# Kernel tuning notes

Hardware: AMD Instinct MI355X
Metric: run time of the kernel (lower is better)

## Reference

```python
import jax, jax.numpy as jnp
import numpy as np

B, T = 4096, 2048
CLIP = 1.0e5


def _hv(x):
    # smooth Heaviside: ~0 for x<0, ~1 for x>0
    return (jnp.tanh(5.0 * x) + 1.0) * 0.5


def setup_inputs() -> dict:
    key = jax.random.key(0)
    k1, _ = jax.random.split(key)
    # columns: prcp, tmean, dayl (all in [0,1) like normalized forcings)
    inputs = jax.random.uniform(k1, (B, T, 3), dtype=jnp.float32)
    # 15 scalar bucket parameters, all initialized to 0.5 as in build():
    # f, smax, qmax, ddf, tmin, tmax, Kc, SCmax, spmax, qpmax, kp, sgmax, qgmax, Kl, Kn
    theta = jnp.full((15,), 0.5, dtype=jnp.float32)
    return {"inputs": inputs, "theta": theta}


def _run(inputs, theta):
    f, smax, qmax, ddf, tmin, tmax, Kc, SCmax, spmax, qpmax, kp, sgmax, qgmax, Kl, Kn = [
        theta[i] for i in range(15)
    ]
    prcp = inputs[:, :, 0]   # [B,T]
    tmean = inputs[:, :, 1]
    dayl = inputs[:, :, 2]
    # Hamon-style PET computed once for the whole sequence
    pet = 29.8 * (dayl * 24.0) * 0.611 * jnp.exp(17.3 * tmean / (tmean + 237.3)) / (tmean + 273.2)

    # rescaled parameters (done once; constant over time)
    f_ = f / 10.0
    smax_ = smax * 1950.0
    qmax_ = qmax * 50.0
    ddf_ = ddf * 5.0
    tmin_ = tmin * -3.0
    tmax_ = tmax * 3.0
    Kc_ = Kc * 0.5
    SCmax_ = SCmax * 1.5
    spmax_ = spmax * 1950.0
    qpmax_ = qpmax * 40.0
    sgmax_ = sgmax * 1950.0
    qgmax_ = qgmax * 40.0
    Kl_ = Kl * 0.5
    Kn_ = Kn * 0.5
    Dc = 0.986 * 0.862

    def step(state, xt):
        s0, s1, s2, s3, s4 = [state[:, i] for i in range(5)]  # each [B]
        p, t, dl, pe = xt  # each [B]

        # canopy bucket
        day = _hv(dl - 0.5)
        night = _hv(0.5 - dl)
        scmax_t = day * SCmax_ * 2.0 + night * SCmax_ * 0.6
        lai_t = day * 0.478 + night * 0.15
        kc_t = day * Kc_ + night * Kc_ * 0.4
        pintc = (_hv(p - 0.1) * _hv(s0) * _hv(s0 - scmax_t) * p
                 + _hv(p - 0.1) * _hv(scmax_t - s0) * kc_t * Dc * lai_t)

        # rain/snow partition
        psnow = _hv(tmin_ - t) * p
        prain = _hv(t - tmin_) * p

        # snow bucket
        melt = _hv(t - tmax_) * _hv(s1) * jnp.minimum(s1, ddf_ * (t - tmax_))

        # preferential bucket
        qpref = (_hv(s2) * _hv(s2 - spmax_) * qpmax_
                 + _hv(s2) * _hv(spmax_ - s2) * kp * p * jnp.exp(-f_ * (spmax_ - s2)))

        # capillary (soil) bucket
        et = (_hv(s3) * _hv(s3 - smax_) * pe
              + _hv(s3) * _hv(smax_ - s3) * pe * (s3 / smax_))
        qsub = (_hv(s3) * _hv(s3 - smax_) * qmax_
                + _hv(s3) * _hv(smax_ - s3) * qmax_ * jnp.exp(-f_ * (smax_ - s3)))
        qout = _hv(s3) * _hv(s3 - smax_) * (s3 - smax_)

        # gravity bucket
        qslow = (_hv(s4) * _hv(s4 - sgmax_) * qgmax_
                 + _hv(s4) * _hv(sgmax_ - s4) * (p * Kl_ + p * p * Kn_) * jnp.exp(-f_ * (sgmax_ - s4)))

        ns0 = s0 + jnp.clip(pintc, -CLIP, CLIP)
        ns1 = s1 + jnp.clip(psnow - melt, -CLIP, CLIP)
        ns2 = s2 + jnp.clip(qpref, -CLIP, CLIP)
        ns3 = s3 + jnp.clip(prain + melt - et - qsub - qout, -CLIP, CLIP)
        ns4 = s4 + jnp.clip(qslow, -CLIP, CLIP)
        new_state = jnp.stack([ns0, ns1, ns2, ns3, ns4], axis=1)  # [B,5]
        return new_state, new_state

    init = jnp.zeros((inputs.shape[0], 5), dtype=inputs.dtype)
    xs = (prcp.T, tmean.T, dayl.T, pet.T)  # time-major [T,B]
    _, seq = jax.lax.scan(step, init, xs)  # seq: [T,B,5]
    return jnp.transpose(seq, (1, 0, 2))  # [B,T,5] state trajectories


def reference(inputs, theta):
    return _run(inputs, theta)
```

## Files before the change

### kernel.cpp

```cpp
#include <hip/hip_runtime.h>


#define NB 4096
#define NT 2048
#define CHUNK 32
#define NCHUNK (NT / CHUNK)
#define K1 16
#define NCH1 (NT / K1)
#define BT ((size_t)NB * (size_t)NT)

#define L2E10 14.4269504089f
#define L2E    1.44269504089f

__device__ __forceinline__ float rcpf(float x) { return __builtin_amdgcn_rcpf(x); }
__device__ __forceinline__ float ex2(float a)  { return __builtin_amdgcn_exp2f(a); }
__device__ __forceinline__ float ex2c(float a) { return __builtin_amdgcn_exp2f(fminf(a, 80.0f)); }
__device__ __forceinline__ float clip1e5(float x) {
    return __builtin_amdgcn_fmed3f(x, -100000.0f, 100000.0f);
}
__device__ __forceinline__ void pinbuf(const float* d, int n4) {
    const float4* v = (const float4*)d;
    #pragma unroll
    for (int i = 0; i < n4; ++i)
        asm volatile("" :: "v"(v[i].x), "v"(v[i].y), "v"(v[i].z), "v"(v[i].w));
}

__global__ __launch_bounds__(256)
void pre_kernel(const float* __restrict__ inp, const float* __restrict__ theta,
                float* __restrict__ scr) {
    const float ddf_  = theta[3] * 5.0f;
    const float tmin_ = theta[4] * -3.0f;
    const float tmax_ = theta[5] * 3.0f;
    const float c_sn  = -L2E10 * tmin_;
    const float c_m   =  L2E10 * tmax_;
    const float c_dd  = -ddf_ * tmax_;

    const size_t k = (size_t)blockIdx.x * 256 + threadIdx.x;
    const float p  = inp[k * 3 + 0];
    const float tm = inp[k * 3 + 1];
    const float dl = inp[k * 3 + 2];

    const float A1 = tm + 237.3f;
    const float A2 = tm + 273.2f;
    const float q  = rcpf(A1 * A2);
    const float pe = 436.98672f * dl * ex2(24.958624f * tm * (q * A2)) * (q * A1);
    const float psnow = rcpf(1.0f + ex2(fmaf(L2E10, tm, c_sn))) * p;
    const float prain = p - psnow;
    const float dm  = 1.0f + ex2(fmaf(-L2E10, tm, c_m));
    const float mdd = fmaf(ddf_, tm, c_dd);

    scr[0 * BT + k] = pe;
    scr[1 * BT + k] = psnow;
    scr[2 * BT + k] = prain;
    scr[3 * BT + k] = dm;
    scr[4 * BT + k] = mdd;
}

__global__ __launch_bounds__(64, 1)
void prnn_roles(const float* __restrict__ inp, const float* __restrict__ theta,
                float* __restrict__ out, float* __restrict__ wsp, int use_ws) {
    const int lane = threadIdx.x;
    const int role = blockIdx.x & 3;
    const int b = (blockIdx.x >> 2) * 64 + lane;

    const float f_     = theta[0] * 0.1f;
    const float smax_  = theta[1] * 1950.0f;
    const float qmax_  = theta[2] * 50.0f;
    const float ddf_   = theta[3] * 5.0f;
    const float tmin_  = theta[4] * -3.0f;
    const float tmax_  = theta[5] * 3.0f;
    const float Kc_    = theta[6] * 0.5f;
    const float SCmax_ = theta[7] * 1.5f;
    const float spmax_ = theta[8] * 1950.0f;
    const float qpmax_ = theta[9] * 40.0f;
    const float kp     = theta[10];
    const float sgmax_ = theta[11] * 1950.0f;
    const float qgmax_ = theta[12] * 40.0f;
    const float Kl_    = theta[13] * 0.5f;
    const float Kn_    = theta[14] * 0.5f;

    const float inv_smax = rcpf(smax_);
    const float KcDc  = Kc_ * 0.849932f;
    const float c_sn  = -L2E10 * tmin_;
    const float c_m   =  L2E10 * tmax_;
    const float c_dd  = -ddf_ * tmax_;
    const float c_sc1 =  L2E10 * SCmax_ * 1.4f;
    const float c_sc0 =  L2E10 * SCmax_ * 0.6f;
    const float c_2p  =  L2E10 * spmax_;
    const float c_3s  =  L2E10 * smax_;
    const float c_4s  =  L2E10 * sgmax_;
    const float fE    = f_ * L2E;
    const float c_E2  = -fE * spmax_;
    const float c_E3  = -fE * smax_;
    const float c_E4  = -fE * sgmax_;

    const float* ip = inp + (size_t)b * (NT * 3);
    float*       op = out + (size_t)b * (NT * 5);
    float* wbase = use_ws ? wsp : out;

    auto plane_storeN = [&](float* plane, const float* ob, int off, int n4) {
        float4* d = (float4*)(plane + (size_t)off);
        const float4* s = (const float4*)ob;
        #pragma unroll
        for (int i = 0; i < 8; ++i) { if (i < n4) d[i] = s[i]; }
    };

    if (role == 0) {
        float s0 = 0.f;
        float bA[CHUNK * 3], bB[CHUNK * 3];
        float* w0 = wbase + 0 * BT + (size_t)b * NT;
        auto pf = [&](float* d, int c) {
            const float4* s = (const float4*)(ip + (size_t)c * (CHUNK * 3));
            #pragma unroll
            for (int i = 0; i < (CHUNK * 3) / 4; ++i) ((float4*)d)[i] = s[i];
        };
        auto cw = [&](const float* d, int c) {
            float ob[CHUNK];
            #pragma unroll
            for (int i = 0; i < CHUNK; ++i) {
                const float p  = d[i * 3 + 0];
                const float dl = d[i * 3 + 2];
                const float day = rcpf(1.0f + ex2(fmaf(-L2E10, dl, 7.21347520f)));
                const float da  = 1.0f + ex2(fmaf(-L2E10, p, L2E));
                const float lai   = fmaf(0.328f, day, 0.15f);
                const float kcf   = fmaf(0.6f, day, 0.4f);
                const float kterm = KcDc * kcf * lai;
                const float zday  = fmaf(c_sc1, day, c_sc0);
                const float e0  = ex2(-L2E10 * s0);
                const float esc = ex2(fmaf(-L2E10, s0, zday));
                const float d0  = 1.0f + e0;
                const float dsc = 1.0f + esc;
                const float Rp  = rcpf(da * d0 * dsc);
                const float pintc = Rp * fmaf(d0 * esc, kterm, p);
                s0 += clip1e5(pintc);
                ob[i] = s0;
            }
            if (use_ws) plane_storeN(w0, ob, c * CHUNK, CHUNK / 4);
            else {
                #pragma unroll
                for (int i = 0; i < CHUNK; ++i) op[(c * CHUNK + i) * 5 + 0] = ob[i];
            }
        };
        pf(bA, 0);
        for (int c = 0; c < NCHUNK; c += 2) {
            pf(bB, c + 1);
            pinbuf(bA, (CHUNK * 3) / 4);
            cw(bA, c);
            if (c + 2 < NCHUNK) pf(bA, c + 2);
            pinbuf(bB, (CHUNK * 3) / 4);
            cw(bB, c + 1);
        }
    } else if (role == 1) {
        float s1 = 0.f, s3 = 0.f;
        float* w1 = wbase + 1 * BT + (size_t)b * NT;
        float* w3 = wbase + 3 * BT + (size_t)b * NT;
        if (use_ws) {
            const float* PE = out + 0 * BT + (size_t)b * NT;
            const float* PS = out + 1 * BT + (size_t)b * NT;
            const float* PR = out + 2 * BT + (size_t)b * NT;
            const float* DM = out + 3 * BT + (size_t)b * NT;
            const float* MD = out + 4 * BT + (size_t)b * NT;
            float peA[K1], psA[K1], prA[K1], dmA[K1], mdA[K1];
            float peB[K1], psB[K1], prB[K1], dmB[K1], mdB[K1];
            float ob1[2 * K1], ob3[2 * K1];
            auto pf = [&](float* pe_, float* ps_, float* pr_, float* dm_,
                          float* md_, int c) {
                const int o = c * K1;
                #pragma unroll
                for (int i = 0; i < K1 / 4; ++i) {
                    ((float4*)pe_)[i] = *(const float4*)(PE + o + i * 4);
                    ((float4*)ps_)[i] = *(const float4*)(PS + o + i * 4);
                    ((float4*)pr_)[i] = *(const float4*)(PR + o + i * 4);
                    ((float4*)dm_)[i] = *(const float4*)(DM + o + i * 4);
                    ((float4*)md_)[i] = *(const float4*)(MD + o + i * 4);
                }
            };
            auto pin5 = [&](const float* pe_, const float* ps_, const float* pr_,
                            const float* dm_, const float* md_) {
                pinbuf(pe_, K1 / 4); pinbuf(ps_, K1 / 4); pinbuf(pr_, K1 / 4);
                pinbuf(dm_, K1 / 4); pinbuf(md_, K1 / 4);
            };
            auto cw = [&](const float* pe_, const float* ps_, const float* pr_,
                          const float* dm_, const float* md_, int half) {
                #pragma unroll
                for (int i = 0; i < K1; ++i) {
                    const float pe = pe_[i], psnow = ps_[i], prain = pr_[i];
                    const float dm = dm_[i], mdd = md_[i];
                    const float e1 = ex2(-L2E10 * s1);
                    const float melt = rcpf(dm * (1.0f + e1)) * fminf(s1, mdd);
                    const float e3  = ex2(-L2E10 * s3);
                    const float e3s = ex2c(fmaf(-L2E10, s3, c_3s));
                    const float R3  = rcpf((1.0f + e3) * (1.0f + e3s));
                    const float E3  = ex2(fmaf(fE, s3, c_E3));
                    const float t_et = pe * fmaf(e3s * s3, inv_smax, 1.0f);
                    const float t_qs = qmax_ * fmaf(e3s, E3, 1.0f);
                    const float outflux = R3 * (t_et + t_qs + (s3 - smax_));
                    const float ds3 = prain + melt - outflux;
                    s1 += clip1e5(psnow - melt);
                    s3 += clip1e5(ds3);
                    ob1[half * K1 + i] = s1;
                    ob3[half * K1 + i] = s3;
                }
            };
            pf(peA, psA, prA, dmA, mdA, 0);
            for (int c = 0; c < NCH1; c += 2) {
                pf(peB, psB, prB, dmB, mdB, c + 1);
                pin5(peA, psA, prA, dmA, mdA);
                cw(peA, psA, prA, dmA, mdA, 0);
                if (c + 2 < NCH1) pf(peA, psA, prA, dmA, mdA, c + 2);
                pin5(peB, psB, prB, dmB, mdB);
                cw(peB, psB, prB, dmB, mdB, 1);
                plane_storeN(w1, ob1, c * K1, (2 * K1) / 4);
                plane_storeN(w3, ob3, c * K1, (2 * K1) / 4);
            }
        } else {
            float bA[CHUNK * 3], bB[CHUNK * 3];
            auto pf = [&](float* d, int c) {
                const float4* s = (const float4*)(ip + (size_t)c * (CHUNK * 3));
                #pragma unroll
                for (int i = 0; i < (CHUNK * 3) / 4; ++i) ((float4*)d)[i] = s[i];
            };
            auto cw = [&](const float* d, int c) {
                #pragma unroll
                for (int i = 0; i < CHUNK; ++i) {
                    const float p  = d[i * 3 + 0];
                    const float tm = d[i * 3 + 1];
                    const float dl = d[i * 3 + 2];
                    const float A1 = tm + 237.3f;
                    const float A2 = tm + 273.2f;
                    const float qq = rcpf(A1 * A2);
                    const float pe = 436.98672f * dl * ex2(24.958624f * tm * (qq * A2)) * (qq * A1);
                    const float psnow = rcpf(1.0f + ex2(fmaf(L2E10, tm, c_sn))) * p;
                    const float dm = 1.0f + ex2(fmaf(-L2E10, tm, c_m));
                    const float prain = p - psnow;
                    const float e1 = ex2(-L2E10 * s1);
                    const float melt = rcpf(dm * (1.0f + e1))
                                       * fminf(s1, fmaf(ddf_, tm, c_dd));
                    const float e3  = ex2(-L2E10 * s3);
                    const float e3s = ex2c(fmaf(-L2E10, s3, c_3s));
                    const float R3  = rcpf((1.0f + e3) * (1.0f + e3s));
                    const float E3  = ex2(fmaf(fE, s3, c_E3));
                    const float t_et = pe * fmaf(e3s * s3, inv_smax, 1.0f);
                    const float t_qs = qmax_ * fmaf(e3s, E3, 1.0f);
                    const float outflux = R3 * (t_et + t_qs + (s3 - smax_));
                    const float ds3 = prain + melt - outflux;
                    s1 += clip1e5(psnow - melt);
                    s3 += clip1e5(ds3);
                    const int t = c * CHUNK + i;
                    op[t * 5 + 1] = s1;
                    op[t * 5 + 3] = s3;
                }
            };
            pf(bA, 0);
            for (int c = 0; c < NCHUNK; c += 2) {
                pf(bB, c + 1);
                pinbuf(bA, (CHUNK * 3) / 4);
                cw(bA, c);
                if (c + 2 < NCHUNK) pf(bA, c + 2);
                pinbuf(bB, (CHUNK * 3) / 4);
                cw(bB, c + 1);
            }
        }
    } else if (role == 2) {
        float s2 = 0.f;
        float pA[CHUNK], pB[CHUNK];
        float* w2 = wbase + 2 * BT + (size_t)b * NT;
        auto pf = [&](float* P, int c) {
            #pragma unroll
            for (int i = 0; i < CHUNK; ++i) P[i] = ip[(c * CHUNK + i) * 3 + 0];
        };
        auto cw = [&](const float* P, int c) {
            float ob[CHUNK];
            #pragma unroll
            for (int i = 0; i < CHUNK; ++i) {
                const float p = P[i];
                const float e2  = ex2(-L2E10 * s2);
                const float e2p = ex2c(fmaf(-L2E10, s2, c_2p));
                const float R2  = rcpf((1.0f + e2) * (1.0f + e2p));
                const float E2  = ex2(fmaf(fE, s2, c_E2));
                const float qpref = R2 * fmaf(e2p * E2, kp * p, qpmax_);
                s2 += clip1e5(qpref);
                ob[i] = s2;
            }
            if (use_ws) plane_storeN(w2, ob, c * CHUNK, CHUNK / 4);
            else {
                #pragma unroll
                for (int i = 0; i < CHUNK; ++i) op[(c * CHUNK + i) * 5 + 2] = ob[i];
            }
        };
        pf(pA, 0);
        for (int c = 0; c < NCHUNK; c += 2) {
            pf(pB, c + 1);
            pinbuf(pA, CHUNK / 4);
            cw(pA, c);
            if (c + 2 < NCHUNK) pf(pA, c + 2);
            pinbuf(pB, CHUNK / 4);
            cw(pB, c + 1);
        }
    } else {
        float s4 = 0.f;
        float pA[CHUNK], pB[CHUNK];
        float* w4 = wbase + 4 * BT + (size_t)b * NT;
        auto pf = [&](float* P, int c) {
            #pragma unroll
            for (int i = 0; i < CHUNK; ++i) P[i] = ip[(c * CHUNK + i) * 3 + 0];
        };
        auto cw = [&](const float* P, int c) {
            float ob[CHUNK];
            #pragma unroll
            for (int i = 0; i < CHUNK; ++i) {
                const float p = P[i];
                const float e4  = ex2(-L2E10 * s4);
                const float e4s = ex2c(fmaf(-L2E10, s4, c_4s));
                const float R4  = rcpf((1.0f + e4) * (1.0f + e4s));
                const float E4  = ex2(fmaf(fE, s4, c_E4));
                const float pl  = p * fmaf(p, Kn_, Kl_);
                const float qslow = R4 * fmaf(e4s * E4, pl, qgmax_);
                s4 += clip1e5(qslow);
                ob[i] = s4;
            }
            if (use_ws) plane_storeN(w4, ob, c * CHUNK, CHUNK / 4);
            else {
                #pragma unroll
                for (int i = 0; i < CHUNK; ++i) op[(c * CHUNK + i) * 5 + 4] = ob[i];
            }
        };
        pf(pA, 0);
        for (int c = 0; c < NCHUNK; c += 2) {
            pf(pB, c + 1);
            pinbuf(pA, CHUNK / 4);
            cw(pA, c);
            if (c + 2 < NCHUNK) pf(pA, c + 2);
            pinbuf(pB, CHUNK / 4);
            cw(pB, c + 1);
        }
    }
}

__global__ __launch_bounds__(256)
void tx_kernel(const float* __restrict__ wsp, float* __restrict__ out) {
    const size_t idx = (size_t)blockIdx.x * 256 + threadIdx.x;
    const size_t b  = idx / (NT / 4);
    const size_t t0 = (idx % (NT / 4)) * 4;
    const float* base = wsp + b * NT + t0;
    const float4 v0 = *(const float4*)(base + 0 * BT);
    const float4 v1 = *(const float4*)(base + 1 * BT);
    const float4 v2 = *(const float4*)(base + 2 * BT);
    const float4 v3 = *(const float4*)(base + 3 * BT);
    const float4 v4 = *(const float4*)(base + 4 * BT);
    float4* o = (float4*)(out + (b * NT + t0) * 5);
    o[0] = make_float4(v0.x, v1.x, v2.x, v3.x);
    o[1] = make_float4(v4.x, v0.y, v1.y, v2.y);
    o[2] = make_float4(v3.y, v4.y, v0.z, v1.z);
    o[3] = make_float4(v2.z, v3.z, v4.z, v0.w);
    o[4] = make_float4(v1.w, v2.w, v3.w, v4.w);
}

extern "C" void kernel_launch(void* const* d_in, const int* in_sizes, int n_in,
                              void* d_out, int out_size, void* d_ws, size_t ws_size,
                              hipStream_t stream) {
    const float* inp   = (const float*)d_in[0];
    const float* theta = (const float*)d_in[1];
    float* out = (float*)d_out;
    float* wsp = (float*)d_ws;
    const int use_ws = (wsp != nullptr && ws_size >= 5 * sizeof(float) * BT) ? 1 : 0;
    if (use_ws)
        pre_kernel<<<(int)(BT / 256), 256, 0, stream>>>(inp, theta, out);
    prnn_roles<<<4 * (NB / 64), 64, 0, stream>>>(inp, theta, out, wsp, use_ws);
    if (use_ws)
        tx_kernel<<<(int)(BT / 4 / 256), 256, 0, stream>>>(wsp, out);
}
```

Before: 567.5 us.

## Pack precomputed forcings into float4 layout and offload canopy terms to pre-kernel

The pre-kernel now processes four timesteps per thread with vector loads. It writes interleaved float4 records (pe, psnow, dm, mdd) plus a contiguous precipitation plane, instead of five separate planes. When the workspace is large enough, it also precomputes the canopy-bucket terms (kterm, zday, da) so role 0's serial recurrence no longer evaluates them per step. Roles 2 and 3 read precipitation from the contiguous plane rather than a strided gather from the input. Chunk sizes also change per role. The cost is extra global traffic and workspace use from the added precomputed planes.

```diff
diff --git a/kernel.cpp b/kernel.cpp
--- a/kernel.cpp
+++ b/kernel.cpp
@@ -3,10 +3,9 @@
 
 #define NB 4096
 #define NT 2048
-#define CHUNK 32
-#define NCHUNK (NT / CHUNK)
+#define CH0 16
 #define K1 16
-#define NCH1 (NT / K1)
+#define CH23 32
 #define BT ((size_t)NB * (size_t)NT)
 
 #define L2E10 14.4269504089f
@@ -27,38 +26,65 @@
 
 __global__ __launch_bounds__(256)
 void pre_kernel(const float* __restrict__ inp, const float* __restrict__ theta,
-                float* __restrict__ scr) {
-    const float ddf_  = theta[3] * 5.0f;
-    const float tmin_ = theta[4] * -3.0f;
-    const float tmax_ = theta[5] * 3.0f;
+                float* __restrict__ out, float* __restrict__ wsp, int use_p0) {
+    const float ddf_   = theta[3] * 5.0f;
+    const float tmin_  = theta[4] * -3.0f;
+    const float tmax_  = theta[5] * 3.0f;
+    const float Kc_    = theta[6] * 0.5f;
+    const float SCmax_ = theta[7] * 1.5f;
+    const float KcDc  = Kc_ * 0.849932f;
     const float c_sn  = -L2E10 * tmin_;
     const float c_m   =  L2E10 * tmax_;
     const float c_dd  = -ddf_ * tmax_;
+    const float c_sc1 =  L2E10 * SCmax_ * 1.4f;
+    const float c_sc0 =  L2E10 * SCmax_ * 0.6f;
 
     const size_t k = (size_t)blockIdx.x * 256 + threadIdx.x;
-    const float p  = inp[k * 3 + 0];
-    const float tm = inp[k * 3 + 1];
-    const float dl = inp[k * 3 + 2];
-
-    const float A1 = tm + 237.3f;
-    const float A2 = tm + 273.2f;
-    const float q  = rcpf(A1 * A2);
-    const float pe = 436.98672f * dl * ex2(24.958624f * tm * (q * A2)) * (q * A1);
-    const float psnow = rcpf(1.0f + ex2(fmaf(L2E10, tm, c_sn))) * p;
-    const float prain = p - psnow;
-    const float dm  = 1.0f + ex2(fmaf(-L2E10, tm, c_m));
-    const float mdd = fmaf(ddf_, tm, c_dd);
-
-    scr[0 * BT + k] = pe;
-    scr[1 * BT + k] = psnow;
-    scr[2 * BT + k] = prain;
-    scr[3 * BT + k] = dm;
-    scr[4 * BT + k] = mdd;
+    const float4* i4 = (const float4*)(inp + k * 12);
+    const float4 A = i4[0], Bv = i4[1], C = i4[2];
+    const float P[4] = {A.x, A.w, Bv.z, C.y};
+    const float T[4] = {A.y, Bv.x, Bv.w, C.z};
+    const float D[4] = {A.z, Bv.y, C.x, C.w};
+
+    float4 pk1[4], pk0[4];
+    float pp[4];
+    #pragma unroll
+    for (int j = 0; j < 4; ++j) {
+        const float p = P[j], tm = T[j], dl = D[j];
+        const float A1 = tm + 237.3f;
+        const float A2 = tm + 273.2f;
+        const float q  = rcpf(A1 * A2);
+        const float pe = 436.98672f * dl * ex2(24.958624f * tm * (q * A2)) * (q * A1);
+        const float psnow = rcpf(1.0f + ex2(fmaf(L2E10, tm, c_sn))) * p;
+        const float dm  = 1.0f + ex2(fmaf(-L2E10, tm, c_m));
+        const float mdd = fmaf(ddf_, tm, c_dd);
+        pk1[j] = make_float4(pe, psnow, dm, mdd);
+        pp[j] = p;
+        if (use_p0) {
+            const float day = rcpf(1.0f + ex2(fmaf(-L2E10, dl, 7.21347520f)));
+            const float da  = 1.0f + ex2(fmaf(-L2E10, p, L2E));
+            const float lai   = fmaf(0.328f, day, 0.15f);
+            const float kcf   = fmaf(0.6f, day, 0.4f);
+            const float kterm = KcDc * kcf * lai;
+            const float zday  = fmaf(c_sc1, day, c_sc0);
+            pk0[j] = make_float4(p, kterm, zday, da);
+        }
+    }
+    float4* o1 = (float4*)out + k * 4;
+    #pragma unroll
+    for (int j = 0; j < 4; ++j) o1[j] = pk1[j];
+    *(float4*)(out + 4 * BT + k * 4) = make_float4(pp[0], pp[1], pp[2], pp[3]);
+    if (use_p0) {
+        float4* o0 = (float4*)(wsp + 5 * BT) + k * 4;
+        #pragma unroll
+        for (int j = 0; j < 4; ++j) o0[j] = pk0[j];
+    }
 }
 
 __global__ __launch_bounds__(64, 1)
 void prnn_roles(const float* __restrict__ inp, const float* __restrict__ theta,
-                float* __restrict__ out, float* __restrict__ wsp, int use_ws) {
+                float* __restrict__ out, float* __restrict__ wsp,
+                int use_ws, int use_p0) {
     const int lane = threadIdx.x;
     const int role = blockIdx.x & 3;
     const int b = (blockIdx.x >> 2) * 64 + lane;
@@ -107,85 +133,112 @@
 
     if (role == 0) {
         float s0 = 0.f;
-        float bA[CHUNK * 3], bB[CHUNK * 3];
         float* w0 = wbase + 0 * BT + (size_t)b * NT;
-        auto pf = [&](float* d, int c) {
-            const float4* s = (const float4*)(ip + (size_t)c * (CHUNK * 3));
-            #pragma unroll
-            for (int i = 0; i < (CHUNK * 3) / 4; ++i) ((float4*)d)[i] = s[i];
-        };
-        auto cw = [&](const float* d, int c) {
-            float ob[CHUNK];
-            #pragma unroll
-            for (int i = 0; i < CHUNK; ++i) {
-                const float p  = d[i * 3 + 0];
-                const float dl = d[i * 3 + 2];
-                const float day = rcpf(1.0f + ex2(fmaf(-L2E10, dl, 7.21347520f)));
-                const float da  = 1.0f + ex2(fmaf(-L2E10, p, L2E));
-                const float lai   = fmaf(0.328f, day, 0.15f);
-                const float kcf   = fmaf(0.6f, day, 0.4f);
-                const float kterm = KcDc * kcf * lai;
-                const float zday  = fmaf(c_sc1, day, c_sc0);
-                const float e0  = ex2(-L2E10 * s0);
-                const float esc = ex2(fmaf(-L2E10, s0, zday));
-                const float d0  = 1.0f + e0;
-                const float dsc = 1.0f + esc;
-                const float Rp  = rcpf(da * d0 * dsc);
-                const float pintc = Rp * fmaf(d0 * esc, kterm, p);
-                s0 += clip1e5(pintc);
-                ob[i] = s0;
-            }
-            if (use_ws) plane_storeN(w0, ob, c * CHUNK, CHUNK / 4);
-            else {
-                #pragma unroll
-                for (int i = 0; i < CHUNK; ++i) op[(c * CHUNK + i) * 5 + 0] = ob[i];
-            }
-        };
-        pf(bA, 0);
-        for (int c = 0; c < NCHUNK; c += 2) {
-            pf(bB, c + 1);
-            pinbuf(bA, (CHUNK * 3) / 4);
-            cw(bA, c);
-            if (c + 2 < NCHUNK) pf(bA, c + 2);
-            pinbuf(bB, (CHUNK * 3) / 4);
-            cw(bB, c + 1);
+        if (use_ws && use_p0) {
+            const float4* PK = (const float4*)(wsp + 5 * BT) + (size_t)b * NT;
+            float bA[CH0 * 4], bB[CH0 * 4];
+            auto pf = [&](float* d, int c) {
+                #pragma unroll
+                for (int i = 0; i < CH0; ++i)
+                    ((float4*)d)[i] = PK[(size_t)c * CH0 + i];
+            };
+            auto cw = [&](const float* d, int c) {
+                float ob[CH0];
+                #pragma unroll
+                for (int i = 0; i < CH0; ++i) {
+                    const float p     = d[i * 4 + 0];
+                    const float kterm = d[i * 4 + 1];
+                    const float zday  = d[i * 4 + 2];
+                    const float da    = d[i * 4 + 3];
+                    const float e0  = ex2(-L2E10 * s0);
+                    const float esc = ex2(fmaf(-L2E10, s0, zday));
+                    const float d0  = 1.0f + e0;
+                    const float dsc = 1.0f + esc;
+                    const float Rp  = rcpf(da * d0 * dsc);
+                    const float pintc = Rp * fmaf(d0 * esc, kterm, p);
+                    s0 += clip1e5(pintc);
+                    ob[i] = s0;
+                }
+                plane_storeN(w0, ob, c * CH0, CH0 / 4);
+            };
+            pf(bA, 0);
+            for (int c = 0; c < NT / CH0; c += 2) {
+                pf(bB, c + 1);
+                pinbuf(bA, CH0);
+                cw(bA, c);
+                if (c + 2 < NT / CH0) pf(bA, c + 2);
+                pinbuf(bB, CH0);
+                cw(bB, c + 1);
+            }
+        } else {
+            float bA[CH0 * 3], bB[CH0 * 3];
+            auto pf = [&](float* d, int c) {
+                const float4* s = (const float4*)(ip + (size_t)c * (CH0 * 3));
+                #pragma unroll
+                for (int i = 0; i < (CH0 * 3) / 4; ++i) ((float4*)d)[i] = s[i];
+            };
+            auto cw = [&](const float* d, int c) {
+                float ob[CH0];
+                #pragma unroll
+                for (int i = 0; i < CH0; ++i) {
+                    const float p  = d[i * 3 + 0];
+                    const float dl = d[i * 3 + 2];
+                    const float day = rcpf(1.0f + ex2(fmaf(-L2E10, dl, 7.21347520f)));
+                    const float da  = 1.0f + ex2(fmaf(-L2E10, p, L2E));
+                    const float lai   = fmaf(0.328f, day, 0.15f);
+                    const float kcf   = fmaf(0.6f, day, 0.4f);
+                    const float kterm = KcDc * kcf * lai;
+                    const float zday  = fmaf(c_sc1, day, c_sc0);
+                    const float e0  = ex2(-L2E10 * s0);
+                    const float esc = ex2(fmaf(-L2E10, s0, zday));
+                    const float d0  = 1.0f + e0;
+                    const float dsc = 1.0f + esc;
+                    const float Rp  = rcpf(da * d0 * dsc);
+                    const float pintc = Rp * fmaf(d0 * esc, kterm, p);
+                    s0 += clip1e5(pintc);
+                    ob[i] = s0;
+                }
+                if (use_ws) plane_storeN(w0, ob, c * CH0, CH0 / 4);
+                else {
+                    #pragma unroll
+                    for (int i = 0; i < CH0; ++i) op[(c * CH0 + i) * 5 + 0] = ob[i];
+                }
+            };
+            pf(bA, 0);
+            for (int c = 0; c < NT / CH0; c += 2) {
+                pf(bB, c + 1);
+                pinbuf(bA, (CH0 * 3) / 4);
+                cw(bA, c);
+                if (c + 2 < NT / CH0) pf(bA, c + 2);
+                pinbuf(bB, (CH0 * 3) / 4);
+                cw(bB, c + 1);
+            }
         }
     } else if (role == 1) {
         float s1 = 0.f, s3 = 0.f;
         float* w1 = wbase + 1 * BT + (size_t)b * NT;
         float* w3 = wbase + 3 * BT + (size_t)b * NT;
         if (use_ws) {
-            const float* PE = out + 0 * BT + (size_t)b * NT;
-            const float* PS = out + 1 * BT + (size_t)b * NT;
-            const float* PR = out + 2 * BT + (size_t)b * NT;
-            const float* DM = out + 3 * BT + (size_t)b * NT;
-            const float* MD = out + 4 * BT + (size_t)b * NT;
-            float peA[K1], psA[K1], prA[K1], dmA[K1], mdA[K1];
-            float peB[K1], psB[K1], prB[K1], dmB[K1], mdB[K1];
+            const float4* PK = (const float4*)out + (size_t)b * NT;
+            const float*  PP = out + 4 * BT + (size_t)b * NT;
+            float kA[K1 * 4], kB[K1 * 4], pA[K1], pB[K1];
             float ob1[2 * K1], ob3[2 * K1];
-            auto pf = [&](float* pe_, float* ps_, float* pr_, float* dm_,
-                          float* md_, int c) {
-                const int o = c * K1;
-                #pragma unroll
-                for (int i = 0; i < K1 / 4; ++i) {
-                    ((float4*)pe_)[i] = *(const float4*)(PE + o + i * 4);
-                    ((float4*)ps_)[i] = *(const float4*)(PS + o + i * 4);
-                    ((float4*)pr_)[i] = *(const float4*)(PR + o + i * 4);
-                    ((float4*)dm_)[i] = *(const float4*)(DM + o + i * 4);
-                    ((float4*)md_)[i] = *(const float4*)(MD + o + i * 4);
-                }
-            };
-            auto pin5 = [&](const float* pe_, const float* ps_, const float* pr_,
-                            const float* dm_, const float* md_) {
-                pinbuf(pe_, K1 / 4); pinbuf(ps_, K1 / 4); pinbuf(pr_, K1 / 4);
-                pinbuf(dm_, K1 / 4); pinbuf(md_, K1 / 4);
-            };
-            auto cw = [&](const float* pe_, const float* ps_, const float* pr_,
-                          const float* dm_, const float* md_, int half) {
+            auto pf = [&](float* kd, float* pd, int c) {
+                #pragma unroll
+                for (int i = 0; i < K1; ++i)
+                    ((float4*)kd)[i] = PK[(size_t)c * K1 + i];
+                #pragma unroll
+                for (int i = 0; i < K1 / 4; ++i)
+                    ((float4*)pd)[i] = *(const float4*)(PP + (size_t)c * K1 + i * 4);
+            };
+            auto cw = [&](const float* kd, const float* pd, int half) {
                 #pragma unroll
                 for (int i = 0; i < K1; ++i) {
-                    const float pe = pe_[i], psnow = ps_[i], prain = pr_[i];
-                    const float dm = dm_[i], mdd = md_[i];
+                    const float pe    = kd[i * 4 + 0];
+                    const float psnow = kd[i * 4 + 1];
+                    const float dm    = kd[i * 4 + 2];
+                    const float mdd   = kd[i * 4 + 3];
+                    const float prain = pd[i] - psnow;
                     const float e1 = ex2(-L2E10 * s1);
                     const float melt = rcpf(dm * (1.0f + e1)) * fminf(s1, mdd);
                     const float e3  = ex2(-L2E10 * s3);
@@ -202,27 +255,27 @@
                     ob3[half * K1 + i] = s3;
                 }
             };
-            pf(peA, psA, prA, dmA, mdA, 0);
-            for (int c = 0; c < NCH1; c += 2) {
-                pf(peB, psB, prB, dmB, mdB, c + 1);
-                pin5(peA, psA, prA, dmA, mdA);
-                cw(peA, psA, prA, dmA, mdA, 0);
-                if (c + 2 < NCH1) pf(peA, psA, prA, dmA, mdA, c + 2);
-                pin5(peB, psB, prB, dmB, mdB);
-                cw(peB, psB, prB, dmB, mdB, 1);
+            pf(kA, pA, 0);
+            for (int c = 0; c < NT / K1; c += 2) {
+                pf(kB, pB, c + 1);
+                pinbuf(kA, K1); pinbuf(pA, K1 / 4);
+                cw(kA, pA, 0);
+                if (c + 2 < NT / K1) pf(kA, pA, c + 2);
+                pinbuf(kB, K1); pinbuf(pB, K1 / 4);
+                cw(kB, pB, 1);
                 plane_storeN(w1, ob1, c * K1, (2 * K1) / 4);
                 plane_storeN(w3, ob3, c * K1, (2 * K1) / 4);
             }
         } else {
-            float bA[CHUNK * 3], bB[CHUNK * 3];
+            float bA[CH0 * 3], bB[CH0 * 3];
             auto pf = [&](float* d, int c) {
-                const float4* s = (const float4*)(ip + (size_t)c * (CHUNK * 3));
-                #pragma unroll
-                for (int i = 0; i < (CHUNK * 3) / 4; ++i) ((float4*)d)[i] = s[i];
+                const float4* s = (const float4*)(ip + (size_t)c * (CH0 * 3));
+                #pragma unroll
+                for (int i = 0; i < (CH0 * 3) / 4; ++i) ((float4*)d)[i] = s[i];
             };
             auto cw = [&](const float* d, int c) {
                 #pragma unroll
-                for (int i = 0; i < CHUNK; ++i) {
+                for (int i = 0; i < CH0; ++i) {
                     const float p  = d[i * 3 + 0];
                     const float tm = d[i * 3 + 1];
                     const float dl = d[i * 3 + 2];
@@ -246,33 +299,40 @@
                     const float ds3 = prain + melt - outflux;
                     s1 += clip1e5(psnow - melt);
                     s3 += clip1e5(ds3);
-                    const int t = c * CHUNK + i;
+                    const int t = c * CH0 + i;
                     op[t * 5 + 1] = s1;
                     op[t * 5 + 3] = s3;
                 }
             };
             pf(bA, 0);
-            for (int c = 0; c < NCHUNK; c += 2) {
+            for (int c = 0; c < NT / CH0; c += 2) {
                 pf(bB, c + 1);
-                pinbuf(bA, (CHUNK * 3) / 4);
+                pinbuf(bA, (CH0 * 3) / 4);
                 cw(bA, c);
-                if (c + 2 < NCHUNK) pf(bA, c + 2);
-                pinbuf(bB, (CHUNK * 3) / 4);
+                if (c + 2 < NT / CH0) pf(bA, c + 2);
+                pinbuf(bB, (CH0 * 3) / 4);
                 cw(bB, c + 1);
             }
         }
     } else if (role == 2) {
         float s2 = 0.f;
-        float pA[CHUNK], pB[CHUNK];
+        float pA[CH23], pB[CH23];
         float* w2 = wbase + 2 * BT + (size_t)b * NT;
+        const float* PP = out + 4 * BT + (size_t)b * NT;
         auto pf = [&](float* P, int c) {
-            #pragma unroll
-            for (int i = 0; i < CHUNK; ++i) P[i] = ip[(c * CHUNK + i) * 3 + 0];
+            if (use_ws) {
+                #pragma unroll
+                for (int i = 0; i < CH23 / 4; ++i)
+                    ((float4*)P)[i] = *(const float4*)(PP + (size_t)c * CH23 + i * 4);
+            } else {
+                #pragma unroll
+                for (int i = 0; i < CH23; ++i) P[i] = ip[(c * CH23 + i) * 3 + 0];
+            }
         };
         auto cw = [&](const float* P, int c) {
-            float ob[CHUNK];
+            float ob[CH23];
             #pragma unroll
-            for (int i = 0; i < CHUNK; ++i) {
+            for (int i = 0; i < CH23; ++i) {
                 const float p = P[i];
                 const float e2  = ex2(-L2E10 * s2);
                 const float e2p = ex2c(fmaf(-L2E10, s2, c_2p));
@@ -282,33 +342,40 @@
                 s2 += clip1e5(qpref);
                 ob[i] = s2;
             }
-            if (use_ws) plane_storeN(w2, ob, c * CHUNK, CHUNK / 4);
+            if (use_ws) plane_storeN(w2, ob, c * CH23, CH23 / 4);
             else {
                 #pragma unroll
-                for (int i = 0; i < CHUNK; ++i) op[(c * CHUNK + i) * 5 + 2] = ob[i];
+                for (int i = 0; i < CH23; ++i) op[(c * CH23 + i) * 5 + 2] = ob[i];
             }
         };
         pf(pA, 0);
-        for (int c = 0; c < NCHUNK; c += 2) {
+        for (int c = 0; c < NT / CH23; c += 2) {
             pf(pB, c + 1);
-            pinbuf(pA, CHUNK / 4);
+            pinbuf(pA, CH23 / 4);
             cw(pA, c);
-            if (c + 2 < NCHUNK) pf(pA, c + 2);
-            pinbuf(pB, CHUNK / 4);
+            if (c + 2 < NT / CH23) pf(pA, c + 2);
+            pinbuf(pB, CH23 / 4);
             cw(pB, c + 1);
         }
     } else {
         float s4 = 0.f;
-        float pA[CHUNK], pB[CHUNK];
+        float pA[CH23], pB[CH23];
         float* w4 = wbase + 4 * BT + (size_t)b * NT;
+        const float* PP = out + 4 * BT + (size_t)b * NT;
         auto pf = [&](float* P, int c) {
-            #pragma unroll
-            for (int i = 0; i < CHUNK; ++i) P[i] = ip[(c * CHUNK + i) * 3 + 0];
+            if (use_ws) {
+                #pragma unroll
+                for (int i = 0; i < CH23 / 4; ++i)
+                    ((float4*)P)[i] = *(const float4*)(PP + (size_t)c * CH23 + i * 4);
+            } else {
+                #pragma unroll
+                for (int i = 0; i < CH23; ++i) P[i] = ip[(c * CH23 + i) * 3 + 0];
+            }
         };
         auto cw = [&](const float* P, int c) {
-            float ob[CHUNK];
+            float ob[CH23];
             #pragma unroll
-            for (int i = 0; i < CHUNK; ++i) {
+            for (int i = 0; i < CH23; ++i) {
                 const float p = P[i];
                 const float e4  = ex2(-L2E10 * s4);
                 const float e4s = ex2c(fmaf(-L2E10, s4, c_4s));
@@ -319,19 +386,19 @@
                 s4 += clip1e5(qslow);
                 ob[i] = s4;
             }
-            if (use_ws) plane_storeN(w4, ob, c * CHUNK, CHUNK / 4);
+            if (use_ws) plane_storeN(w4, ob, c * CH23, CH23 / 4);
             else {
                 #pragma unroll
-                for (int i = 0; i < CHUNK; ++i) op[(c * CHUNK + i) * 5 + 4] = ob[i];
+                for (int i = 0; i < CH23; ++i) op[(c * CH23 + i) * 5 + 4] = ob[i];
             }
         };
         pf(pA, 0);
-        for (int c = 0; c < NCHUNK; c += 2) {
+        for (int c = 0; c < NT / CH23; c += 2) {
             pf(pB, c + 1);
-            pinbuf(pA, CHUNK / 4);
+            pinbuf(pA, CH23 / 4);
             cw(pA, c);
-            if (c + 2 < NCHUNK) pf(pA, c + 2);
-            pinbuf(pB, CHUNK / 4);
+            if (c + 2 < NT / CH23) pf(pA, c + 2);
+            pinbuf(pB, CH23 / 4);
             cw(pB, c + 1);
         }
     }
@@ -364,9 +431,10 @@
     float* out = (float*)d_out;
     float* wsp = (float*)d_ws;
     const int use_ws = (wsp != nullptr && ws_size >= 5 * sizeof(float) * BT) ? 1 : 0;
+    const int use_p0 = (wsp != nullptr && ws_size >= 9 * sizeof(float) * BT) ? 1 : 0;
     if (use_ws)
-        pre_kernel<<<(int)(BT / 256), 256, 0, stream>>>(inp, theta, out);
-    prnn_roles<<<4 * (NB / 64), 64, 0, stream>>>(inp, theta, out, wsp, use_ws);
+        pre_kernel<<<(int)(BT / 4 / 256), 256, 0, stream>>>(inp, theta, out, wsp, use_p0);
+    prnn_roles<<<4 * (NB / 64), 64, 0, stream>>>(inp, theta, out, wsp, use_ws, use_p0);
     if (use_ws)
         tx_kernel<<<(int)(BT / 4 / 256), 256, 0, stream>>>(wsp, out);
 }
```

Result: slower. 617.2 us (+8.8%).
